# Kernel tuning notes

Hardware: AMD Instinct MI355X
Metric: run time of the kernel (lower is better)

Reference implementation:

```python
import jax, jax.numpy as jnp
import numpy as np

D_MODEL = 512
D_STATE = 64
L_SEQ = 4096
BATCH = 4


def _make_A(N):
    # HiPPO-LegS style A: A[n,k] = -sqrt(2n+1)sqrt(2k+1) if n>k, -(n+1) if n==k, 0 else (n,k from 1..N)
    idx = np.arange(1, N + 1, dtype=np.float64)
    M = np.sqrt(2 * idx[:, None] + 1) * np.sqrt(2 * idx[None, :] + 1)
    lower = (idx[:, None] > idx[None, :]).astype(np.float64)
    return -(lower * M + np.diag(idx + 1))


def _discretize(A, B, C, step):
    # bilinear (Tustin) transform
    I = np.eye(A.shape[0])
    BL = np.linalg.inv(I - step / 2.0 * A)
    Ab = BL @ (I + step / 2.0 * A)
    Bb = (BL * step) @ B
    return Ab, Bb, C


def setup_inputs() -> dict:
    key = jax.random.key(0)
    rng = np.random.RandomState(0)
    A = _make_A(D_STATE)
    B = rng.randn(D_STATE, 1)
    C = rng.randn(1, D_STATE)
    Ab, Bb, Cb = _discretize(A, B, C, step=1.0 / L_SEQ)
    u = jax.random.normal(key, (BATCH, L_SEQ, D_MODEL), dtype=jnp.float32)
    return {
        "u": u,
        "A_": jnp.asarray(Ab, dtype=jnp.float32),
        "B_": jnp.asarray(Bb, dtype=jnp.float32),
        "C_": jnp.asarray(Cb, dtype=jnp.float32),
    }


def reference(u, A_, B_, C_):
    # u: (B, L, D) -> flatten channels: (BD, L)
    b, L, d = u.shape
    uc = u.transpose(0, 2, 1).reshape(b * d, L)
    N = A_.shape[0]
    b_vec = B_[:, 0]  # (N,)
    c_vec = C_[0]     # (N,)

    def step(x, u_k):
        # x: (BD, N), u_k: (BD,)
        # x_k = A_ @ x_{k-1}^T + B_ @ u_k^T  (expressed batched as x @ A_.T + outer)
        x_new = x @ A_.T + u_k[:, None] * b_vec[None, :]
        y_k = x_new @ c_vec  # (BD,)
        return x_new, y_k

    x0 = jnp.zeros((b * d, N), dtype=u.dtype)
    _, ys = jax.lax.scan(step, x0, uc.T)  # ys: (L, BD)
    y = ys.T.reshape(b, d, L).transpose(0, 2, 1)  # (B, L, D)
    return y
```

## Files before the change

kernel.cpp:

```cpp
#include <hip/hip_runtime.h>

#define L_SEQ   4096
#define D_MODEL 512
#define NSEQ    2048
#define CH      128
#define NC      32

#define OFF_P    0
#define OFF_W1T  4096
#define OFF_WOUT 12288
#define OFF_KLOC 20480
#define OFF_KZ3  20736
#define OFF_GX   21760

#define BC(v, j) __int_as_float(__builtin_amdgcn_readlane(__float_as_int(v), (j)))

__global__ __launch_bounds__(1024) void k_prep(
    const float* __restrict__ A, const float* __restrict__ B,
    const float* __restrict__ C, float* __restrict__ ws) {
  __shared__ float Srow[64][68];
  __shared__ float STs[64][68];
  __shared__ float vrT[128][68];
  __shared__ float cwS[129][68];
  __shared__ float Cs[64], Bsh[64];
  __shared__ float KzSh[256];

  const int tid = threadIdx.x;
  if (tid < 64) { Cs[tid] = C[tid]; Bsh[tid] = B[tid]; }
  for (int e = tid; e < 4096; e += 1024) {
    const float a = A[e];
    Srow[e >> 6][e & 63] = a;
    STs[e & 63][e >> 6] = a;
  }
  __syncthreads();

  if (tid < 64) {
    vrT[0][tid] = Bsh[tid];
    float acc = 0.f;
#pragma unroll
    for (int k = 0; k < 64; ++k) acc += Cs[k] * STs[tid][k];
    cwS[1][tid] = acc;
  }
  __syncthreads();

  const bool sq = (tid >= 768);
  const int stid = tid & 255;
  const int iy4 = (stid >> 4) * 4, jx4 = (stid & 15) * 4;

  for (int t = 0; t < 7; ++t) {
    const int nd = 1 << t;

    if (nd <= 2) {
      const int total = 2 * nd * 64;
      if (tid < total) {
        const int half = (tid >= nd * 64);
        const int o = (tid >> 6) & (nd - 1);
        const int idx = tid & 63;
        float acc = 0.f;
        if (!half) {
#pragma unroll
          for (int k = 0; k < 64; ++k) acc += vrT[o][k] * Srow[idx][k];
          vrT[nd + o][idx] = acc;
        } else {
#pragma unroll
          for (int k = 0; k < 64; ++k) acc += cwS[1 + o][k] * STs[idx][k];
          cwS[nd + 1 + o][idx] = acc;
        }
      }
    } else {
      const int tpg = nd * 4;
      if (tid < 2 * tpg) {
        const int half = (tid >= tpg);
        const int q = half ? tid - tpg : tid;
        const int m0 = (q >> 4) * 4;
        const int i0 = (q & 15) * 4;
        float acc[4][4] = {{0.f}};
        if (!half) {
#pragma unroll 4
          for (int k = 0; k < 64; k += 4) {
            float a_[4][4];
#pragma unroll
            for (int r = 0; r < 4; ++r)
              *(float4*)&a_[r][0] = *(const float4*)&vrT[m0 + r][k];
#pragma unroll
            for (int kk = 0; kk < 4; ++kk) {
              const float4 b4 = *(const float4*)&STs[k + kk][i0];
#pragma unroll
              for (int r = 0; r < 4; ++r) {
                const float av = a_[r][kk];
                acc[r][0] += av * b4.x; acc[r][1] += av * b4.y;
                acc[r][2] += av * b4.z; acc[r][3] += av * b4.w;
              }
            }
          }
#pragma unroll
          for (int r = 0; r < 4; ++r) {
            float4 v; v.x = acc[r][0]; v.y = acc[r][1]; v.z = acc[r][2]; v.w = acc[r][3];
            *(float4*)&vrT[nd + m0 + r][i0] = v;
          }
        } else {
#pragma unroll 4
          for (int k = 0; k < 64; k += 4) {
            float a_[4][4];
#pragma unroll
            for (int r = 0; r < 4; ++r)
              *(float4*)&a_[r][0] = *(const float4*)&cwS[1 + m0 + r][k];
#pragma unroll
            for (int kk = 0; kk < 4; ++kk) {
              const float4 b4 = *(const float4*)&Srow[k + kk][i0];
#pragma unroll
              for (int r = 0; r < 4; ++r) {
                const float av = a_[r][kk];
                acc[r][0] += av * b4.x; acc[r][1] += av * b4.y;
                acc[r][2] += av * b4.z; acc[r][3] += av * b4.w;
              }
            }
          }
#pragma unroll
          for (int r = 0; r < 4; ++r) {
            float4 v; v.x = acc[r][0]; v.y = acc[r][1]; v.z = acc[r][2]; v.w = acc[r][3];
            *(float4*)&cwS[nd + 1 + m0 + r][i0] = v;
          }
        }
      }
    }

    float sacc[4][4] = {{0.f}};
    if (sq) {
#pragma unroll 4
      for (int k = 0; k < 64; k += 4) {
        float a_[4][4];
#pragma unroll
        for (int r = 0; r < 4; ++r)
          *(float4*)&a_[r][0] = *(const float4*)&Srow[iy4 + r][k];
#pragma unroll
        for (int kk = 0; kk < 4; ++kk) {
          const float4 b4 = *(const float4*)&Srow[k + kk][jx4];
#pragma unroll
          for (int r = 0; r < 4; ++r) {
            const float av = a_[r][kk];
            sacc[r][0] += av * b4.x; sacc[r][1] += av * b4.y;
            sacc[r][2] += av * b4.z; sacc[r][3] += av * b4.w;
          }
        }
      }
    }
    __syncthreads();
    if (sq) {
#pragma unroll
      for (int r = 0; r < 4; ++r) {
        float4 v; v.x = sacc[r][0]; v.y = sacc[r][1]; v.z = sacc[r][2]; v.w = sacc[r][3];
        *(float4*)&Srow[iy4 + r][jx4] = v;
      }
#pragma unroll
      for (int c = 0; c < 4; ++c) {
        float4 v; v.x = sacc[0][c]; v.y = sacc[1][c]; v.z = sacc[2][c]; v.w = sacc[3][c];
        *(float4*)&STs[jx4 + c][iy4] = v;
      }
    }
    __syncthreads();
  }

  float* Pg = ws + OFF_P;
  for (int e = tid; e < 4096; e += 1024) Pg[e] = Srow[e >> 6][e & 63];

  float* W1Tg = ws + OFF_W1T;
  for (int e = tid; e < 8192; e += 1024) W1Tg[e] = vrT[127 - (e >> 6)][e & 63];

  float* Wg = ws + OFF_WOUT;
  for (int e = tid; e < 8192; e += 1024) Wg[e] = cwS[(e & 127) + 1][e >> 7];

  float* Kz = ws + OFF_KLOC;
  if (tid < 128) {
    float acc = 0.f;
#pragma unroll
    for (int i = 0; i < 64; ++i) acc += Cs[i] * vrT[tid][i];
    KzSh[128 + tid] = acc;
    Kz[128 + tid] = acc;
  } else if (tid < 256) {
    KzSh[tid - 128] = 0.f;
    Kz[tid - 128] = 0.f;
  }
  __syncthreads();

  float* Kz3g = ws + OFF_KZ3;
  if (tid < 264) Kz3g[tid] = (tid >= 3 && tid < 259) ? KzSh[tid - 3] : 0.f;
}

__global__ __launch_bounds__(256) void k_proj(
    const float* __restrict__ u, const float* __restrict__ wsr,
    float* __restrict__ gx) {
  __shared__ float Us[64][64];

  const int st = blockIdx.x;
  const int c = blockIdx.y;
  const int tid = threadIdx.x;
  const int sgl = st * 64;
  const int bi = sgl >> 9, d0 = sgl & 511;

  const float* W1Tg = wsr + OFF_W1T;
  const float* ub = u + ((size_t)bi * L_SEQ + c * CH) * D_MODEL + d0;
  const int sy4 = (tid >> 4) * 4;
  const int ix4 = (tid & 15) * 4;

  float acc[4][4];
#pragma unroll
  for (int r = 0; r < 4; ++r)
#pragma unroll
    for (int cc = 0; cc < 4; ++cc) acc[r][cc] = 0.f;

  for (int h = 0; h < 2; ++h) {
    __syncthreads();
#pragma unroll
    for (int e4 = 0; e4 < 4; ++e4) {
      const int e = tid + 256 * e4;
      const int rr = e >> 4, s4 = (e & 15) * 4;
      *(float4*)&Us[rr][s4] =
          *(const float4*)(ub + (size_t)(h * 64 + rr) * D_MODEL + s4);
    }
    __syncthreads();
#pragma unroll 8
    for (int kk = 0; kk < 64; ++kk) {
      const float4 a = *(const float4*)&Us[kk][sy4];
      const float4 b =
          *(const float4*)(W1Tg + (size_t)(h * 64 + kk) * 64 + ix4);
      const float av[4] = {a.x, a.y, a.z, a.w};
      const float bv[4] = {b.x, b.y, b.z, b.w};
#pragma unroll
      for (int ii = 0; ii < 4; ++ii)
#pragma unroll
        for (int jj = 0; jj < 4; ++jj) acc[ii][jj] += av[ii] * bv[jj];
    }
  }

  float* gb = gx + ((size_t)c * NSEQ + sgl) * 64;
#pragma unroll
  for (int j = 0; j < 4; ++j) {
    float4 v; v.x = acc[j][0]; v.y = acc[j][1]; v.z = acc[j][2]; v.w = acc[j][3];
    *(float4*)(gb + (size_t)(sy4 + j) * 64 + ix4) = v;
  }
}

__global__ __launch_bounds__(256) void k_scan(
    const float* __restrict__ wsr, float* __restrict__ gx) {
  const int lane = threadIdx.x & 63, wv = threadIdx.x >> 6;
  const int s = blockIdx.x * 4 + wv;

  float p[64];
  {
    const float* pr = wsr + OFF_P + lane * 64;
#pragma unroll
    for (int j = 0; j < 64; j += 4) {
      const float4 v = *(const float4*)(pr + j);
      p[j] = v.x; p[j + 1] = v.y; p[j + 2] = v.z; p[j + 3] = v.w;
    }
  }

  const size_t CS = (size_t)NSEQ * 64;
  float* gs = gx + (size_t)s * 64 + lane;
  float x = 0.f;
  float g0 = gs[0];
  float g1 = gs[CS];
  float g2 = gs[2 * CS];
  float g3 = gs[3 * CS];
  for (int c = 0; c < NC; ++c) {
    const float gn = (c + 4 < NC) ? gs[(size_t)(c + 4) * CS] : 0.f;
    gs[(size_t)c * CS] = x;
    float x0 = g0, x1 = 0.f;
#pragma unroll
    for (int j = 0; j < 64; j += 2) {
      x0 += p[j] * BC(x, j);
      x1 += p[j + 1] * BC(x, j + 1);
    }
    x = x0 + x1;
    g0 = g1; g1 = g2; g2 = g3; g3 = gn;
  }
}

#define LB(k, s)   LDSf[(k) * 64 + (s)]
#define LKZ3       4096

__global__ __launch_bounds__(256) void k_localout(
    const float* __restrict__ u, const float* __restrict__ wsr,
    const float* __restrict__ gx, float* __restrict__ out) {
  __shared__ float LDSf[5200];

  const int sg = blockIdx.x;
  const int c = blockIdx.y;
  const int sgl = sg * 64;
  const int bi = sgl >> 9, d0 = sgl & 511;

  const float* Kz3g = wsr + OFF_KZ3;
  const float* WoutG = wsr + OFF_WOUT;
  const float* ub = u + ((size_t)bi * L_SEQ + c * CH) * D_MODEL + d0;

  const int tid = threadIdx.x;
  const int ry8 = (tid >> 4) * 8;
  const int sx4 = (tid & 15) * 4;

  if (tid < 66) {
    const float4 v = *(const float4*)(Kz3g + tid * 4);
#pragma unroll
    for (int q = 0; q < 4; ++q)
      *(float4*)&LDSf[LKZ3 + q * 276 + tid * 4] = v;
  }

  float acc[8][4];
#pragma unroll
  for (int r = 0; r < 8; ++r)
#pragma unroll
    for (int cc = 0; cc < 4; ++cc) acc[r][cc] = 0.f;

  const float* lkz = &LDSf[LKZ3 + ((tid >> 4) & 3) * 276];

  for (int kt = 0; kt < 2; ++kt) {
    const int k0 = kt * 64;
#pragma unroll
    for (int e4 = 0; e4 < 4; ++e4) {
      const int e = tid + 256 * e4;
      const int kk = e >> 4, s4 = (e & 15) * 4;
      *(float4*)&LB(kk, s4) =
          *(const float4*)(ub + (size_t)(k0 + kk) * D_MODEL + s4);
    }
    __syncthreads();
    const int base = 128 - k0;
    if (kt == 0 || ry8 >= 64) {
#pragma unroll 4
      for (int g = 0; g < 16; ++g) {
        const int Wg = base + ry8 - 4 * g;
        const float4 w0 = *(const float4*)&lkz[Wg];
        const float4 w1 = *(const float4*)&lkz[Wg + 4];
        const float4 w2 = *(const float4*)&lkz[Wg + 8];
        const float w[12] = {w0.x, w0.y, w0.z, w0.w, w1.x, w1.y, w1.z, w1.w,
                             w2.x, w2.y, w2.z, w2.w};
#pragma unroll
        for (int k2 = 0; k2 < 4; ++k2) {
          const float4 b = *(const float4*)&LB(4 * g + k2, sx4);
          const float bv[4] = {b.x, b.y, b.z, b.w};
#pragma unroll
          for (int ii = 0; ii < 8; ++ii) {
            const float av = w[ii - k2 + 3];
#pragma unroll
            for (int jj = 0; jj < 4; ++jj) acc[ii][jj] += av * bv[jj];
          }
        }
      }
    }
    __syncthreads();
  }

  {
    const float* xc = gx + ((size_t)c * NSEQ + sgl) * 64;
#pragma unroll
    for (int e4 = 0; e4 < 4; ++e4) {
      const int e = tid + 256 * e4;
      const int sl = e & 63, i4 = ((e >> 6) & 15) * 4;
      const float4 v = *(const float4*)(xc + (size_t)sl * 64 + i4);
      LB(i4 + 0, sl) = v.x;
      LB(i4 + 1, sl) = v.y;
      LB(i4 + 2, sl) = v.z;
      LB(i4 + 3, sl) = v.w;
    }
    __syncthreads();
#pragma unroll 8
    for (int kk = 0; kk < 64; ++kk) {
      const float4 a0 = *(const float4*)(WoutG + kk * 128 + ry8);
      const float4 a1 = *(const float4*)(WoutG + kk * 128 + ry8 + 4);
      const float4 b = *(const float4*)&LB(kk, sx4);
      const float av[8] = {a0.x, a0.y, a0.z, a0.w, a1.x, a1.y, a1.z, a1.w};
      const float bv[4] = {b.x, b.y, b.z, b.w};
#pragma unroll
      for (int ii = 0; ii < 8; ++ii)
#pragma unroll
        for (int jj = 0; jj < 4; ++jj) acc[ii][jj] += av[ii] * bv[jj];
    }
  }

  float* ob = out + ((size_t)bi * L_SEQ + c * CH) * D_MODEL + d0;
#pragma unroll
  for (int r = 0; r < 8; ++r) {
    float4 v; v.x = acc[r][0]; v.y = acc[r][1]; v.z = acc[r][2]; v.w = acc[r][3];
    *(float4*)(ob + (size_t)(ry8 + r) * D_MODEL + sx4) = v;
  }
}

extern "C" void kernel_launch(void* const* d_in, const int* in_sizes, int n_in,
                              void* d_out, int out_size, void* d_ws,
                              size_t ws_size, hipStream_t stream) {
  const float* u = (const float*)d_in[0];
  const float* A = (const float*)d_in[1];
  const float* B = (const float*)d_in[2];
  const float* C = (const float*)d_in[3];
  float* out = (float*)d_out;
  float* ws = (float*)d_ws;
  float* gx = ws + OFF_GX;

  k_prep<<<1, 1024, 0, stream>>>(A, B, C, ws);
  k_proj<<<dim3(32, 32), 256, 0, stream>>>(u, ws, gx);
  k_scan<<<512, 256, 0, stream>>>(ws, gx);
  k_localout<<<dim3(32, 32), 256, 0, stream>>>(u, ws, gx, out);
}
```

Before: 192.6 us.

## Split reduction dimension across two thread halves in proj and localout kernels

Both k_proj and k_localout now launch 512 threads per block. The two 256-thread halves each take one half of the reduction (the K dimension), and the partial sums are combined through shared memory before the store. The full 128-row input chunk is loaded in a single stage, which removes the two-pass loop and its barriers. This doubles in-flight waves per tile to hide latency, at the cost of more LDS, an extra reduction pass with barriers, and half the threads sitting idle during the final writeback.

```diff
diff --git a/kernel.cpp b/kernel.cpp
--- a/kernel.cpp
+++ b/kernel.cpp
@@ -187,10 +187,10 @@
   if (tid < 264) Kz3g[tid] = (tid >= 3 && tid < 259) ? KzSh[tid - 3] : 0.f;
 }
 
-__global__ __launch_bounds__(256) void k_proj(
+__global__ __launch_bounds__(512, 8) void k_proj(
     const float* __restrict__ u, const float* __restrict__ wsr,
     float* __restrict__ gx) {
-  __shared__ float Us[64][64];
+  __shared__ float Us[8192];
 
   const int st = blockIdx.x;
   const int c = blockIdx.y;
@@ -200,8 +200,18 @@
 
   const float* W1Tg = wsr + OFF_W1T;
   const float* ub = u + ((size_t)bi * L_SEQ + c * CH) * D_MODEL + d0;
-  const int sy4 = (tid >> 4) * 4;
-  const int ix4 = (tid & 15) * 4;
+  const int q = tid >> 8, stid = tid & 255;
+  const int sy4 = (stid >> 4) * 4;
+  const int ix4 = (stid & 15) * 4;
+
+#pragma unroll
+  for (int e4 = 0; e4 < 4; ++e4) {
+    const int e = tid + 512 * e4;
+    const int rr = e >> 4, s4 = (e & 15) * 4;
+    *(float4*)&Us[rr * 64 + s4] =
+        *(const float4*)(ub + (size_t)rr * D_MODEL + s4);
+  }
+  __syncthreads();
 
   float acc[4][4];
 #pragma unroll
@@ -209,35 +219,39 @@
 #pragma unroll
     for (int cc = 0; cc < 4; ++cc) acc[r][cc] = 0.f;
 
-  for (int h = 0; h < 2; ++h) {
-    __syncthreads();
-#pragma unroll
-    for (int e4 = 0; e4 < 4; ++e4) {
-      const int e = tid + 256 * e4;
-      const int rr = e >> 4, s4 = (e & 15) * 4;
-      *(float4*)&Us[rr][s4] =
-          *(const float4*)(ub + (size_t)(h * 64 + rr) * D_MODEL + s4);
-    }
-    __syncthreads();
+  const int r0 = q * 64;
 #pragma unroll 8
-    for (int kk = 0; kk < 64; ++kk) {
-      const float4 a = *(const float4*)&Us[kk][sy4];
-      const float4 b =
-          *(const float4*)(W1Tg + (size_t)(h * 64 + kk) * 64 + ix4);
-      const float av[4] = {a.x, a.y, a.z, a.w};
-      const float bv[4] = {b.x, b.y, b.z, b.w};
-#pragma unroll
-      for (int ii = 0; ii < 4; ++ii)
-#pragma unroll
-        for (int jj = 0; jj < 4; ++jj) acc[ii][jj] += av[ii] * bv[jj];
-    }
-  }
-
-  float* gb = gx + ((size_t)c * NSEQ + sgl) * 64;
-#pragma unroll
-  for (int j = 0; j < 4; ++j) {
-    float4 v; v.x = acc[j][0]; v.y = acc[j][1]; v.z = acc[j][2]; v.w = acc[j][3];
-    *(float4*)(gb + (size_t)(sy4 + j) * 64 + ix4) = v;
+  for (int rr = 0; rr < 64; ++rr) {
+    const int r = r0 + rr;
+    const float4 a = *(const float4*)&Us[r * 64 + sy4];
+    const float4 b = *(const float4*)(W1Tg + (size_t)r * 64 + ix4);
+    const float av[4] = {a.x, a.y, a.z, a.w};
+    const float bv[4] = {b.x, b.y, b.z, b.w};
+#pragma unroll
+    for (int ii = 0; ii < 4; ++ii)
+#pragma unroll
+      for (int jj = 0; jj < 4; ++jj) acc[ii][jj] += av[ii] * bv[jj];
+  }
+
+  __syncthreads();
+  if (q == 1) {
+#pragma unroll
+    for (int j = 0; j < 4; ++j) {
+      float4 v; v.x = acc[j][0]; v.y = acc[j][1]; v.z = acc[j][2]; v.w = acc[j][3];
+      *(float4*)&Us[(j * 256 + stid) * 4] = v;
+    }
+  }
+  __syncthreads();
+  if (q == 0) {
+    float* gb = gx + ((size_t)c * NSEQ + sgl) * 64;
+#pragma unroll
+    for (int j = 0; j < 4; ++j) {
+      const float4 p = *(const float4*)&Us[(j * 256 + stid) * 4];
+      float4 v;
+      v.x = acc[j][0] + p.x; v.y = acc[j][1] + p.y;
+      v.z = acc[j][2] + p.z; v.w = acc[j][3] + p.w;
+      *(float4*)(gb + (size_t)(sy4 + j) * 64 + ix4) = v;
+    }
   }
 }
 
@@ -278,12 +292,12 @@
 }
 
 #define LB(k, s)   LDSf[(k) * 64 + (s)]
-#define LKZ3       4096
-
-__global__ __launch_bounds__(256) void k_localout(
+#define LKZ3       8192
+
+__global__ __launch_bounds__(512, 8) void k_localout(
     const float* __restrict__ u, const float* __restrict__ wsr,
     const float* __restrict__ gx, float* __restrict__ out) {
-  __shared__ float LDSf[5200];
+  __shared__ float LDSf[9296];
 
   const int sg = blockIdx.x;
   const int c = blockIdx.y;
@@ -295,15 +309,24 @@
   const float* ub = u + ((size_t)bi * L_SEQ + c * CH) * D_MODEL + d0;
 
   const int tid = threadIdx.x;
-  const int ry8 = (tid >> 4) * 8;
-  const int sx4 = (tid & 15) * 4;
-
+  const int q = tid >> 8, stid = tid & 255;
+  const int ry8 = (stid >> 4) * 8;
+  const int sx4 = (stid & 15) * 4;
+
+#pragma unroll
+  for (int e4 = 0; e4 < 4; ++e4) {
+    const int e = tid + 512 * e4;
+    const int kk = e >> 4, s4 = (e & 15) * 4;
+    *(float4*)&LB(kk, s4) =
+        *(const float4*)(ub + (size_t)kk * D_MODEL + s4);
+  }
   if (tid < 66) {
     const float4 v = *(const float4*)(Kz3g + tid * 4);
 #pragma unroll
-    for (int q = 0; q < 4; ++q)
-      *(float4*)&LDSf[LKZ3 + q * 276 + tid * 4] = v;
-  }
+    for (int cp = 0; cp < 4; ++cp)
+      *(float4*)&LDSf[LKZ3 + cp * 276 + tid * 4] = v;
+  }
+  __syncthreads();
 
   float acc[8][4];
 #pragma unroll
@@ -311,49 +334,39 @@
 #pragma unroll
     for (int cc = 0; cc < 4; ++cc) acc[r][cc] = 0.f;
 
-  const float* lkz = &LDSf[LKZ3 + ((tid >> 4) & 3) * 276];
-
-  for (int kt = 0; kt < 2; ++kt) {
-    const int k0 = kt * 64;
-#pragma unroll
-    for (int e4 = 0; e4 < 4; ++e4) {
-      const int e = tid + 256 * e4;
-      const int kk = e >> 4, s4 = (e & 15) * 4;
-      *(float4*)&LB(kk, s4) =
-          *(const float4*)(ub + (size_t)(k0 + kk) * D_MODEL + s4);
-    }
-    __syncthreads();
-    const int base = 128 - k0;
-    if (kt == 0 || ry8 >= 64) {
+  const float* lkz = &LDSf[LKZ3 + ((stid >> 4) & 3) * 276];
+
+  if (q == 0 || ry8 >= 64) {
+    const int g0 = q * 16;
 #pragma unroll 4
-      for (int g = 0; g < 16; ++g) {
-        const int Wg = base + ry8 - 4 * g;
-        const float4 w0 = *(const float4*)&lkz[Wg];
-        const float4 w1 = *(const float4*)&lkz[Wg + 4];
-        const float4 w2 = *(const float4*)&lkz[Wg + 8];
-        const float w[12] = {w0.x, w0.y, w0.z, w0.w, w1.x, w1.y, w1.z, w1.w,
-                             w2.x, w2.y, w2.z, w2.w};
-#pragma unroll
-        for (int k2 = 0; k2 < 4; ++k2) {
-          const float4 b = *(const float4*)&LB(4 * g + k2, sx4);
-          const float bv[4] = {b.x, b.y, b.z, b.w};
-#pragma unroll
-          for (int ii = 0; ii < 8; ++ii) {
-            const float av = w[ii - k2 + 3];
-#pragma unroll
-            for (int jj = 0; jj < 4; ++jj) acc[ii][jj] += av * bv[jj];
-          }
+    for (int gg = 0; gg < 16; ++gg) {
+      const int g = g0 + gg;
+      const int Wg = 128 + ry8 - 4 * g;
+      const float4 w0 = *(const float4*)&lkz[Wg];
+      const float4 w1 = *(const float4*)&lkz[Wg + 4];
+      const float4 w2 = *(const float4*)&lkz[Wg + 8];
+      const float w[12] = {w0.x, w0.y, w0.z, w0.w, w1.x, w1.y, w1.z, w1.w,
+                           w2.x, w2.y, w2.z, w2.w};
+#pragma unroll
+      for (int k2 = 0; k2 < 4; ++k2) {
+        const float4 b = *(const float4*)&LB(4 * g + k2, sx4);
+        const float bv[4] = {b.x, b.y, b.z, b.w};
+#pragma unroll
+        for (int ii = 0; ii < 8; ++ii) {
+          const float av = w[ii - k2 + 3];
+#pragma unroll
+          for (int jj = 0; jj < 4; ++jj) acc[ii][jj] += av * bv[jj];
         }
       }
     }
-    __syncthreads();
-  }
+  }
+  __syncthreads();
 
   {
     const float* xc = gx + ((size_t)c * NSEQ + sgl) * 64;
 #pragma unroll
-    for (int e4 = 0; e4 < 4; ++e4) {
-      const int e = tid + 256 * e4;
+    for (int e2 = 0; e2 < 2; ++e2) {
+      const int e = tid + 512 * e2;
       const int sl = e & 63, i4 = ((e >> 6) & 15) * 4;
       const float4 v = *(const float4*)(xc + (size_t)sl * 64 + i4);
       LB(i4 + 0, sl) = v.x;
@@ -362,25 +375,41 @@
       LB(i4 + 3, sl) = v.w;
     }
     __syncthreads();
+    const int i0 = q * 32;
 #pragma unroll 8
-    for (int kk = 0; kk < 64; ++kk) {
-      const float4 a0 = *(const float4*)(WoutG + kk * 128 + ry8);
-      const float4 a1 = *(const float4*)(WoutG + kk * 128 + ry8 + 4);
-      const float4 b = *(const float4*)&LB(kk, sx4);
+    for (int ii_ = 0; ii_ < 32; ++ii_) {
+      const int i = i0 + ii_;
+      const float4 a0 = *(const float4*)(WoutG + i * 128 + ry8);
+      const float4 a1 = *(const float4*)(WoutG + i * 128 + ry8 + 4);
+      const float4 b = *(const float4*)&LB(i, sx4);
       const float av[8] = {a0.x, a0.y, a0.z, a0.w, a1.x, a1.y, a1.z, a1.w};
       const float bv[4] = {b.x, b.y, b.z, b.w};
 #pragma unroll
-      for (int ii = 0; ii < 8; ++ii)
-#pragma unroll
-        for (int jj = 0; jj < 4; ++jj) acc[ii][jj] += av[ii] * bv[jj];
-    }
-  }
-
-  float* ob = out + ((size_t)bi * L_SEQ + c * CH) * D_MODEL + d0;
-#pragma unroll
-  for (int r = 0; r < 8; ++r) {
-    float4 v; v.x = acc[r][0]; v.y = acc[r][1]; v.z = acc[r][2]; v.w = acc[r][3];
-    *(float4*)(ob + (size_t)(ry8 + r) * D_MODEL + sx4) = v;
+      for (int r = 0; r < 8; ++r)
+#pragma unroll
+        for (int jj = 0; jj < 4; ++jj) acc[r][jj] += av[r] * bv[jj];
+    }
+  }
+
+  __syncthreads();
+  if (q == 1) {
+#pragma unroll
+    for (int j = 0; j < 8; ++j) {
+      float4 v; v.x = acc[j][0]; v.y = acc[j][1]; v.z = acc[j][2]; v.w = acc[j][3];
+      *(float4*)&LDSf[(j * 256 + stid) * 4] = v;
+    }
+  }
+  __syncthreads();
+  if (q == 0) {
+    float* ob = out + ((size_t)bi * L_SEQ + c * CH) * D_MODEL + d0;
+#pragma unroll
+    for (int j = 0; j < 8; ++j) {
+      const float4 p = *(const float4*)&LDSf[(j * 256 + stid) * 4];
+      float4 v;
+      v.x = acc[j][0] + p.x; v.y = acc[j][1] + p.y;
+      v.z = acc[j][2] + p.z; v.w = acc[j][3] + p.w;
+      *(float4*)(ob + (size_t)(ry8 + j) * D_MODEL + sx4) = v;
+    }
   }
 }
 
@@ -396,7 +425,7 @@
   float* gx = ws + OFF_GX;
 
   k_prep<<<1, 1024, 0, stream>>>(A, B, C, ws);
-  k_proj<<<dim3(32, 32), 256, 0, stream>>>(u, ws, gx);
+  k_proj<<<dim3(32, 32), 512, 0, stream>>>(u, ws, gx);
   k_scan<<<512, 256, 0, stream>>>(ws, gx);
-  k_localout<<<dim3(32, 32), 256, 0, stream>>>(u, ws, gx, out);
+  k_localout<<<dim3(32, 32), 512, 0, stream>>>(u, ws, gx, out);
 }
```

New measurement: 204.1 us. 6.0% more time.
